# Kernel tuning notes

Hardware: AMD Instinct MI355X
Metric: run time of the kernel (lower is better)

## Reference

```python
import jax, jax.numpy as jnp
import numpy as np
import math

ANGLE_THRESHOLD = math.radians(5.0)  # angle_threshold_deg=5.0
IQR_SCALE = 1.5
PI = np.pi


def setup_inputs() -> dict:
    key = jax.random.key(0)
    k1, k2 = jax.random.split(key)
    B, N, E = 1, 4096, 4096
    node_positions = jax.random.uniform(k1, (B, N, 2), dtype=jnp.float32) * 100.0
    adjacency = jnp.zeros((B, N, N), dtype=jnp.float32)  # unused by the axiom math
    edge_index = jax.random.randint(k2, (2, E), 0, B * N, dtype=jnp.int32)
    return {"node_positions": node_positions, "adjacency": adjacency, "edge_index": edge_index}


def reference(node_positions, adjacency, edge_index):
    """ParallelPairConstancyAxiom forward -> scalar loss.

    Vectorized equivalent of sort + host while-loop pair sweep: the pair set is
    exactly all (ei < ej) with circular angle distance <= threshold.
    """
    E = edge_index.shape[1]
    pos = node_positions.reshape(-1, 2)                      # (B*N, 2)
    src, dst = edge_index[0], edge_index[1]
    vec = pos[dst] - pos[src]                                # (E, 2)
    length = jnp.maximum(jnp.linalg.norm(vec, axis=-1, keepdims=True), 1e-8)
    dirs = vec / length                                      # normalized directions
    ang = jnp.arctan2(dirs[:, 1], dirs[:, 0]) % PI           # angles in [0, pi)

    # circular angle distance on [0, pi): min(|da|, pi-|da|)
    da = jnp.abs(ang[:, None] - ang[None, :])                # (E, E)
    circ = jnp.minimum(da, PI - da)
    upper = jnp.triu(jnp.ones((E, E), dtype=bool), k=1)      # ei < ej, no self-pairs
    mask = upper & (circ <= ANGLE_THRESHOLD)

    # perpendicular distance from edge i's line to midpoint of edge j
    normal = jnp.stack([-dirs[:, 1], dirs[:, 0]], axis=-1)   # (E, 2)
    mid = (pos[src] + pos[dst]) * 0.5                        # (E, 2)
    c = jnp.sum(pos[src] * normal, axis=-1)                  # (E,)
    dist = jnp.abs(normal @ mid.T - c[:, None])              # (E, E)

    n = jnp.sum(mask)                                        # number of parallel pairs
    sorted_d = jnp.sort(jnp.where(mask, dist, jnp.inf).reshape(-1))
    # torch: q1_idx = max(0, int(n*0.25)-1); q3_idx = min(n-1, int(n*0.75)); mu at n//2
    q1 = sorted_d[jnp.maximum(0, n // 4 - 1)]
    q3 = sorted_d[jnp.minimum(n - 1, (3 * n) // 4)]
    iqr = jnp.maximum(q3 - q1, 1e-6)
    mu = sorted_d[n // 2]
    margin = iqr * 0.5 * IQR_SCALE

    per_pair = jnp.maximum(jnp.abs(dist - mu) - margin, 0.0)
    loss = jnp.sum(jnp.where(mask, per_pair, 0.0)) / jnp.maximum(n, 1).astype(per_pair.dtype)
    return loss
```

## Files before the change

kernel.cpp:

```cpp
#include <hip/hip_runtime.h>
#include <hip/hip_bf16.h>
#include <math.h>

#define E_N 4096
#define PI_F 3.14159265358979323846f
#define ATH 0.08726646259971647f

#define NB1 2048
#define SCALE1 12.8f
#define W1 0.078125f
#define SUMSC 16384.0f
#define MASK44 ((1ull << 44) - 1ull)

#define TILE 128
#define NT   (E_N / TILE)
#define NBLK (NT * (NT + 1) / 2)
#define THR  1024

#define N_HIST 16

#define O_H1  0
#define ZBYTES (N_HIST * NB1 * 8)

__global__ __launch_bounds__(THR) void pair_hist(const void* __restrict__ posv,
                                                 const int* __restrict__ eidx,
                                                 char* __restrict__ ws)
{
    unsigned long long* h1 = (unsigned long long*)(ws + O_H1);

    __shared__ float4 rowA[TILE];
    __shared__ float4 colA[TILE];
    __shared__ unsigned long long s_s64[NB1];
    __shared__ unsigned s_flag;

    int tid = threadIdx.x, bid = blockIdx.x;

    int tr = 0, rem = bid;
    while (rem >= NT - tr) { rem -= NT - tr; ++tr; }
    int tc = tr + rem;

    if (tid == 0) s_flag = 0u;
    for (int k = tid; k < NB1; k += THR) s_s64[k] = 0ull;
    __syncthreads();

    {
        const unsigned short* ph = (const unsigned short*)posv;
        unsigned f = 0;
#pragma unroll
        for (int k = 0; k < 8; ++k) {
            unsigned short v = ph[tid + k * 1024];
            if (((v >> 7) & 0xFFu) >= 137u) f = 1u;
        }
        if (f) atomicOr(&s_flag, 1u);
    }
    __syncthreads();
    bool isf32 = (s_flag != 0u);

    if (tid < 2 * TILE) {
        bool isCol = tid < TILE;
        int local = isCol ? tid : tid - TILE;
        int e = (isCol ? tc : tr) * TILE + local;
        int s = eidx[e], d2 = eidx[E_N + e];
        float px, py, qx, qy;
        if (isf32) {
            const float* pf = (const float*)posv;
            px = pf[2*s]; py = pf[2*s+1]; qx = pf[2*d2]; qy = pf[2*d2+1];
        } else {
            const __hip_bfloat16* pb = (const __hip_bfloat16*)posv;
            px = __bfloat162float(pb[2*s]); py = __bfloat162float(pb[2*s+1]);
            qx = __bfloat162float(pb[2*d2]); qy = __bfloat162float(pb[2*d2+1]);
        }
        float vx = qx - px, vy = qy - py;
        float len = fmaxf(sqrtf(vx*vx + vy*vy), 1e-8f);
        float dx = vx / len, dy = vy / len;
        float a = fmodf(atan2f(dy, dx), PI_F);
        if (a < 0.0f) a += PI_F;
        if (isCol) colA[local] = make_float4(a, (px + qx) * 0.5f, (py + qy) * 0.5f, 0.0f);
        else       rowA[local] = make_float4(a, -dy, dx, px * (-dy) + py * dx);
    }
    __syncthreads();

    {
        int r = tid & (TILE - 1);
        int q = tid >> 7;
        float4 rg = rowA[r];
        float angp = rg.x, nx = rg.y, ny = rg.z, c = rg.w;
        int j0 = q * 16;
        bool diag = (tr == tc);
#pragma unroll 4
        for (int jj = 0; jj < 16; ++jj) {
            int j = j0 + jj;
            if (diag && j <= r) continue;
            float4 cg = colA[j];
            float da = fabsf(angp - cg.x);
            float circ = fminf(da, PI_F - da);
            if (circ <= ATH) {
                float d = fabsf(nx * cg.y + ny * cg.z - c);
                int b = (int)(d * SCALE1); if (b > NB1 - 1) b = NB1 - 1;
                atomicAdd(&s_s64[b],
                          (1ull << 44) | (unsigned long long)(d * SUMSC + 0.5f));
            }
        }
    }
    __syncthreads();

    {
        unsigned long long* myh = h1 + (unsigned)(bid & (N_HIST - 1)) * NB1;
        for (int k = tid; k < NB1; k += THR) {
            unsigned long long v = s_s64[k];
            if (v) atomicAdd(&myh[k], v);
        }
    }
}

__global__ __launch_bounds__(THR) void reduce_ep(const char* __restrict__ ws,
                                                 unsigned* __restrict__ out)
{
    const unsigned long long* h1 = (const unsigned long long*)(ws + O_H1);

    __shared__ unsigned s_scan[THR];
    __shared__ float   s_vv[3];
    __shared__ float   s_lohi[2];
    __shared__ double  s_dw[THR / 64];

    int tid = threadIdx.x;
    int w = tid >> 6, lane = tid & 63;

    unsigned long long v0 = 0ull, v1 = 0ull;
    {
        const ulonglong2* hv = (const ulonglong2*)h1;
#pragma unroll
        for (int c = 0; c < N_HIST; ++c) {
            ulonglong2 p = hv[c * (NB1 / 2) + tid];
            v0 += p.x; v1 += p.y;
        }
    }
    unsigned g0, g1; double S0, S1;
    g0 = (unsigned)(v0 >> 44); g1 = (unsigned)(v1 >> 44);
    S0 = (double)(v0 & MASK44) * (1.0 / 16384.0);
    S1 = (double)(v1 & MASK44) * (1.0 / 16384.0);
    unsigned gs = g0 + g1;
    s_scan[tid] = gs;
    __syncthreads();
    for (int off = 1; off < THR; off <<= 1) {
        unsigned v = (tid >= off) ? s_scan[tid - off] : 0u;
        __syncthreads();
        s_scan[tid] += v;
        __syncthreads();
    }
    unsigned n = s_scan[THR - 1];
    if (n == 0) {
        if (tid == 0) {
            __hip_bfloat16 h = __float2bfloat16(0.0f);
            unsigned short b = *(unsigned short*)&h;
            out[0] = ((unsigned)b << 16) | (unsigned)b;
        }
        return;
    }
    long long q1i = (long long)(n / 4) - 1; if (q1i < 0) q1i = 0;
    long long q3i = (3LL * (long long)n) / 4;
    if (q3i > (long long)n - 1) q3i = (long long)n - 1;
    unsigned rks[3] = { (unsigned)q1i, n / 2, (unsigned)q3i };
    unsigned excl = s_scan[tid] - gs;
    unsigned gl[2] = { g0, g1 };
    for (int t = 0; t < 3; ++t) {
        unsigned r = rks[t];
        if (r >= excl && r < excl + gs) {
            unsigned cum = excl;
#pragma unroll
            for (int k = 0; k < 2; ++k) {
                unsigned c2 = cum + gl[k];
                if (r < c2) {
                    int b = 2 * tid + k;
                    float rr = (float)(r - cum);
                    s_vv[t] = ((float)b + (rr + 0.5f) / (float)gl[k]) * W1;
                    break;
                }
                cum = c2;
            }
        }
    }
    __syncthreads();
    if (tid == 0) {
        float iqr = fmaxf(s_vv[2] - s_vv[0], 1e-6f);
        float mu = s_vv[1];
        float margin = 0.75f * iqr;
        s_lohi[0] = mu - margin;
        s_lohi[1] = mu + margin;
    }
    __syncthreads();
    float lo = s_lohi[0], hi = s_lohi[1];
    double H = 0.0;
#pragma unroll
    for (int k = 0; k < 2; ++k) {
        int b = 2 * tid + k;
        unsigned c = gl[k];
        if (!c) continue;
        double S = k ? S1 : S0;
        float blo = (float)b * W1, bhi = blo + W1;
        if (bhi <= lo) {
            H += (double)lo * (double)c - S;
        } else if (blo >= hi) {
            H += S - (double)hi * (double)c;
        } else {
            double cf = (double)c / (double)W1;
            if (blo < lo) {
                float u1 = fminf(bhi, lo);
                double a0 = (double)lo - (double)blo;
                double a1 = (double)lo - (double)u1;
                H += cf * 0.5 * (a0 * a0 - a1 * a1);
            }
            if (bhi > hi) {
                float v0b = fmaxf(blo, hi);
                double b1 = (double)bhi - (double)hi;
                double b0 = (double)v0b - (double)hi;
                H += cf * 0.5 * (b1 * b1 - b0 * b0);
            }
        }
    }
    for (int off = 32; off > 0; off >>= 1) H += __shfl_down(H, off, 64);
    if (lane == 0) s_dw[w] = H;
    __syncthreads();
    if (tid == 0) {
        double tot = 0.0;
        for (int k = 0; k < THR / 64; ++k) tot += s_dw[k];
        float loss = (float)(tot / (double)n);
        __hip_bfloat16 h = __float2bfloat16(loss);
        unsigned short b = *(unsigned short*)&h;
        out[0] = ((unsigned)b << 16) | (unsigned)b;
    }
}

extern "C" void kernel_launch(void* const* d_in, const int* in_sizes, int n_in,
                              void* d_out, int out_size, void* d_ws, size_t ws_size,
                              hipStream_t stream) {
    const void* pos = d_in[0];
    const int* eidx = (const int*)d_in[2];
    char* ws = (char*)d_ws;
    unsigned* outp = (unsigned*)d_out;

    hipMemsetAsync(ws, 0, ZBYTES, stream);
    pair_hist<<<NBLK, THR, 0, stream>>>(pos, eidx, ws);
    reduce_ep<<<1, THR, 0, stream>>>(ws, outp);
}
```

Baseline: 112.6 us.

## Replace per-block shared histogram with direct global atomics and halve block size

Result: slower. 173.5 us (+54.1%).

```diff
diff --git a/kernel.cpp b/kernel.cpp
--- a/kernel.cpp
+++ b/kernel.cpp
@@ -15,22 +15,22 @@
 #define TILE 128
 #define NT   (E_N / TILE)
 #define NBLK (NT * (NT + 1) / 2)
-#define THR  1024
+#define THR1 512
+#define THR2 1024
 
 #define N_HIST 16
 
 #define O_H1  0
 #define ZBYTES (N_HIST * NB1 * 8)
 
-__global__ __launch_bounds__(THR) void pair_hist(const void* __restrict__ posv,
-                                                 const int* __restrict__ eidx,
-                                                 char* __restrict__ ws)
+__global__ __launch_bounds__(THR1) void pair_hist(const void* __restrict__ posv,
+                                                  const int* __restrict__ eidx,
+                                                  char* __restrict__ ws)
 {
     unsigned long long* h1 = (unsigned long long*)(ws + O_H1);
 
     __shared__ float4 rowA[TILE];
     __shared__ float4 colA[TILE];
-    __shared__ unsigned long long s_s64[NB1];
     __shared__ unsigned s_flag;
 
     int tid = threadIdx.x, bid = blockIdx.x;
@@ -40,15 +40,14 @@
     int tc = tr + rem;
 
     if (tid == 0) s_flag = 0u;
-    for (int k = tid; k < NB1; k += THR) s_s64[k] = 0ull;
     __syncthreads();
 
     {
         const unsigned short* ph = (const unsigned short*)posv;
         unsigned f = 0;
 #pragma unroll
-        for (int k = 0; k < 8; ++k) {
-            unsigned short v = ph[tid + k * 1024];
+        for (int k = 0; k < 16; ++k) {
+            unsigned short v = ph[tid + k * THR1];
             if (((v >> 7) & 0xFFu) >= 137u) f = 1u;
         }
         if (f) atomicOr(&s_flag, 1u);
@@ -85,10 +84,12 @@
         int q = tid >> 7;
         float4 rg = rowA[r];
         float angp = rg.x, nx = rg.y, ny = rg.z, c = rg.w;
-        int j0 = q * 16;
+        int j0 = q * 32;
         bool diag = (tr == tc);
+        unsigned long long* myh =
+            h1 + (unsigned)(((bid << 2) | q) & (N_HIST - 1)) * NB1;
 #pragma unroll 4
-        for (int jj = 0; jj < 16; ++jj) {
+        for (int jj = 0; jj < 32; ++jj) {
             int j = j0 + jj;
             if (diag && j <= r) continue;
             float4 cg = colA[j];
@@ -97,31 +98,22 @@
             if (circ <= ATH) {
                 float d = fabsf(nx * cg.y + ny * cg.z - c);
                 int b = (int)(d * SCALE1); if (b > NB1 - 1) b = NB1 - 1;
-                atomicAdd(&s_s64[b],
+                atomicAdd(&myh[b],
                           (1ull << 44) | (unsigned long long)(d * SUMSC + 0.5f));
             }
         }
     }
-    __syncthreads();
-
-    {
-        unsigned long long* myh = h1 + (unsigned)(bid & (N_HIST - 1)) * NB1;
-        for (int k = tid; k < NB1; k += THR) {
-            unsigned long long v = s_s64[k];
-            if (v) atomicAdd(&myh[k], v);
-        }
-    }
 }
 
-__global__ __launch_bounds__(THR) void reduce_ep(const char* __restrict__ ws,
-                                                 unsigned* __restrict__ out)
+__global__ __launch_bounds__(THR2) void reduce_ep(const char* __restrict__ ws,
+                                                  unsigned* __restrict__ out)
 {
     const unsigned long long* h1 = (const unsigned long long*)(ws + O_H1);
 
-    __shared__ unsigned s_scan[THR];
+    __shared__ unsigned s_scan[THR2];
     __shared__ float   s_vv[3];
     __shared__ float   s_lohi[2];
-    __shared__ double  s_dw[THR / 64];
+    __shared__ double  s_dw[THR2 / 64];
 
     int tid = threadIdx.x;
     int w = tid >> 6, lane = tid & 63;
@@ -142,13 +134,13 @@
     unsigned gs = g0 + g1;
     s_scan[tid] = gs;
     __syncthreads();
-    for (int off = 1; off < THR; off <<= 1) {
+    for (int off = 1; off < THR2; off <<= 1) {
         unsigned v = (tid >= off) ? s_scan[tid - off] : 0u;
         __syncthreads();
         s_scan[tid] += v;
         __syncthreads();
     }
-    unsigned n = s_scan[THR - 1];
+    unsigned n = s_scan[THR2 - 1];
     if (n == 0) {
         if (tid == 0) {
             __hip_bfloat16 h = __float2bfloat16(0.0f);
@@ -223,7 +215,7 @@
     __syncthreads();
     if (tid == 0) {
         double tot = 0.0;
-        for (int k = 0; k < THR / 64; ++k) tot += s_dw[k];
+        for (int k = 0; k < THR2 / 64; ++k) tot += s_dw[k];
         float loss = (float)(tot / (double)n);
         __hip_bfloat16 h = __float2bfloat16(loss);
         unsigned short b = *(unsigned short*)&h;
@@ -240,6 +232,6 @@
     unsigned* outp = (unsigned*)d_out;
 
     hipMemsetAsync(ws, 0, ZBYTES, stream);
-    pair_hist<<<NBLK, THR, 0, stream>>>(pos, eidx, ws);
-    reduce_ep<<<1, THR, 0, stream>>>(ws, outp);
+    pair_hist<<<NBLK, THR1, 0, stream>>>(pos, eidx, ws);
+    reduce_ep<<<1, THR2, 0, stream>>>(ws, outp);
 }
```
